# Kernel optimization log

Hardware: AMD Instinct MI355X
Metric: run time of the kernel (lower is better)

The kernel has to match this reference:

```python
import jax, jax.numpy as jnp
import numpy as np

B, N, F_NODE = 4, 50000, 64
E = 1600000
C, F_COL = 1000, 32
H = 16


def setup_inputs() -> dict:
    key = jax.random.key(0)
    ks = jax.random.split(key, 16)
    s = 0.1
    return {
        "node_features": jax.random.normal(ks[0], (B, N, F_NODE), jnp.float32),
        "col_features": jax.random.normal(ks[1], (B, C, F_COL), jnp.float32),
        "edge_index": jax.random.randint(ks[2], (2, E), 0, N, jnp.int32),
        "W1": jax.random.normal(ks[3], (F_NODE, H), jnp.float32) * s,
        "b1": jnp.zeros((H,), jnp.float32),
        "W2": jax.random.normal(ks[4], (H, H), jnp.float32) * s,
        "b2": jnp.zeros((H,), jnp.float32),
        "node_fc_W": jax.random.normal(ks[5], (H, 1), jnp.float32) * s,
        "node_fc_b": jnp.zeros((1,), jnp.float32),
        "col_W1": jax.random.normal(ks[6], (F_COL, H), jnp.float32) * s,
        "col_b1": jnp.zeros((H,), jnp.float32),
        "col_W2": jax.random.normal(ks[7], (H, 1), jnp.float32) * s,
        "col_b2": jnp.zeros((1,), jnp.float32),
        "fc_W": jax.random.normal(ks[8], (2, H), jnp.float32) * s,
        "fc_b": jnp.zeros((H,), jnp.float32),
        "out_W": jax.random.normal(ks[9], (H, 1), jnp.float32) * s,
        "out_b": jnp.zeros((1,), jnp.float32),
    }


def _gcn_conv(x, src, dst, W, b, num_nodes):
    # PyG GCNConv: x' = D^-1/2 (A+I) D^-1/2 (x W) + b
    x = x @ W
    loops = jnp.arange(num_nodes, dtype=src.dtype)
    s = jnp.concatenate([src, loops])
    d = jnp.concatenate([dst, loops])
    deg = jax.ops.segment_sum(jnp.ones_like(d, x.dtype), d, num_segments=num_nodes)
    dinv = jnp.where(deg > 0, jax.lax.rsqrt(deg), 0.0)
    norm = dinv[s] * dinv[d]                     # [E']
    msg = x[s] * norm[:, None]                   # gather + scale
    out = jax.ops.segment_sum(msg, d, num_segments=num_nodes)  # scatter-add
    return out + b


def reference(node_features, col_features, edge_index, W1, b1, W2, b2,
              node_fc_W, node_fc_b, col_W1, col_b1, col_W2, col_b2,
              fc_W, fc_b, out_W, out_b):
    Bs, Nn, Fn = node_features.shape
    num_nodes = Bs * Nn
    x = node_features.reshape(num_nodes, Fn)
    # faithful to torch: edge_index.expand(B,2,E).reshape(2,-1) (indices NOT offset per batch)
    Ee = edge_index.shape[1]
    ei = jnp.broadcast_to(edge_index, (Bs, 2, Ee)).reshape(2, Bs * Ee)
    src, dst = ei[0], ei[1]
    x = jax.nn.relu(_gcn_conv(x, src, dst, W1, b1, num_nodes))
    x = jax.nn.relu(_gcn_conv(x, src, dst, W2, b2, num_nodes))
    x = x.reshape(Bs, Nn, -1)
    node_out = (x @ node_fc_W + node_fc_b)[..., 0]          # [B, N]
    h = jax.nn.relu(col_features @ col_W1 + col_b1)
    col_out = (h @ col_W2 + col_b2)[..., 0]                 # [B, C]
    node_avg = node_out.mean(axis=1)[:, None]               # [B, 1]
    col_avg = col_out.mean(axis=1)[:, None]                 # [B, 1]
    combined = jnp.concatenate([node_avg, col_avg], axis=1)  # [B, 2]
    z = jax.nn.relu(combined @ fc_W + fc_b)
    return z @ out_W + out_b                                # [B, 1]
```

## Files before the change

kernel.cpp:

```cpp
#include <hip/hip_runtime.h>

static constexpr int NN   = 50000;
static constexpr int NBAT = 4;
static constexpr int NE   = 1600000;
static constexpr int NC   = 1000;
static constexpr int FN   = 64;
static constexpr int FCOL = 32;
static constexpr int HD   = 16;

static constexpr int NP     = 20;
static constexpr int PNODES = 2500;
static constexpr int PCAP   = 88000;
static constexpr int NSUB   = 1000;
static constexpr int SNODES = 50;
static constexpr int SCAP   = 2048;
static constexpr int SPP    = 50;
static constexpr int SLICES = 44;
static constexpr int CHUNK  = 4096;
static constexpr int CHUNK2 = 2048;

static constexpr int P1B  = (NE + CHUNK - 1) / CHUNK;
static constexpr int MLPB = (NN + 127) / 128;
static constexpr int COLB = 16;
static constexpr int MEGAB = P1B + NBAT * MLPB + COLB;

__device__ inline float block_reduce_256(float v) {
    __shared__ float s[4];
    int lane = threadIdx.x & 63, wid = threadIdx.x >> 6;
    #pragma unroll
    for (int o = 32; o > 0; o >>= 1) v += __shfl_down(v, o);
    if (lane == 0) s[wid] = v;
    __syncthreads();
    if (threadIdx.x == 0) {
        float t = 0.f;
        #pragma unroll
        for (int i = 0; i < 4; i++) t += s[i];
        return t;
    }
    return 0.f;
}

__device__ inline float dot4(float4 a, float4 w) {
    return (a.x * w.x + a.y * w.y) + (a.z * w.z + a.w * w.w);
}

__device__ inline float4 quad_reduce_scatter(const float (&p)[16], int q) {
    constexpr int KA[8] = {0,1,2,3,8,9,10,11};
    constexpr int KB[8] = {4,5,6,7,12,13,14,15};
    bool hi1 = (q & 1);
    float m[8];
    #pragma unroll
    for (int i = 0; i < 8; i++) {
        float send = hi1 ? p[KA[i]] : p[KB[i]];
        float recv = __shfl_xor(send, 1);
        m[i] = (hi1 ? p[KB[i]] : p[KA[i]]) + recv;
    }
    bool hi2 = (q & 2);
    float s0 = hi2 ? m[0] : m[4];
    float s1 = hi2 ? m[1] : m[5];
    float s2 = hi2 ? m[2] : m[6];
    float s3 = hi2 ? m[3] : m[7];
    float v0 = __shfl_xor(s0, 2);
    float v1 = __shfl_xor(s1, 2);
    float v2 = __shfl_xor(s2, 2);
    float v3 = __shfl_xor(s3, 2);
    return make_float4((hi2 ? m[4] : m[0]) + v0, (hi2 ? m[5] : m[1]) + v1,
                       (hi2 ? m[6] : m[2]) + v2, (hi2 ? m[7] : m[3]) + v3);
}

__device__ inline float mlp_tail(float4 t, int q, bool valid, const float* sw2,
                                 float4 bv, float4 b2v, float4 nfv) {
    float h0 = fmaxf(t.x + bv.x, 0.f);
    float h1 = fmaxf(t.y + bv.y, 0.f);
    float h2 = fmaxf(t.z + bv.z, 0.f);
    float h3 = fmaxf(t.w + bv.w, 0.f);
    float pk[16];
    const float* r0p = &sw2[(q * 4 + 0) * 20];
    const float* r1p = &sw2[(q * 4 + 1) * 20];
    const float* r2p = &sw2[(q * 4 + 2) * 20];
    const float* r3p = &sw2[(q * 4 + 3) * 20];
    #pragma unroll
    for (int k4 = 0; k4 < 4; k4++) {
        float4 w0 = *(const float4*)&r0p[k4 * 4];
        float4 w1 = *(const float4*)&r1p[k4 * 4];
        float4 w2 = *(const float4*)&r2p[k4 * 4];
        float4 w3 = *(const float4*)&r3p[k4 * 4];
        pk[k4*4+0] = h0 * w0.x + h1 * w1.x + h2 * w2.x + h3 * w3.x;
        pk[k4*4+1] = h0 * w0.y + h1 * w1.y + h2 * w2.y + h3 * w3.y;
        pk[k4*4+2] = h0 * w0.z + h1 * w1.z + h2 * w2.z + h3 * w3.z;
        pk[k4*4+3] = h0 * w0.w + h1 * w1.w + h2 * w2.w + h3 * w3.w;
    }
    float4 f = quad_reduce_scatter(pk, q);
    float sv = fmaxf(f.x + b2v.x, 0.f) * nfv.x
             + fmaxf(f.y + b2v.y, 0.f) * nfv.y
             + fmaxf(f.z + b2v.z, 0.f) * nfv.z
             + fmaxf(f.w + b2v.w, 0.f) * nfv.w;
    return valid ? sv : 0.f;
}

__global__ void __launch_bounds__(256) k_mega(
        const float* __restrict__ x, const int* __restrict__ src,
        const int* __restrict__ dst, const float* __restrict__ col,
        const float* __restrict__ W1, const float* __restrict__ b1,
        const float* __restrict__ W2, const float* __restrict__ b2,
        const float* __restrict__ nfcW,
        const float* __restrict__ cW1, const float* __restrict__ cb1,
        const float* __restrict__ cW2,
        int* __restrict__ gcur, unsigned* __restrict__ buf1,
        float* __restrict__ y1, double* __restrict__ sums) {
    __shared__ int ph[NP], pg[NP], pl[NP];
    __shared__ float swt[HD * FN];
    __shared__ float sw2[HD * 20];
    __shared__ float sb1[HD], sb2[HD], snf[HD];
    __shared__ float cw1s[FCOL * HD], csb1[HD], csw2[HD];

    int tid = threadIdx.x;
    int idx = blockIdx.x;
    int i5 = idx / 5, r5 = idx - i5 * 5;
    bool isP1 = (r5 == 0) && (i5 < P1B);

    if (isP1) {
        if (tid < NP) ph[tid] = 0;
        __syncthreads();
        int e0 = i5 * CHUNK;
        unsigned ent[16]; int bin[16];
        #pragma unroll
        for (int k = 0; k < 16; k++) {
            int e = e0 + k * 256 + tid;
            if (e < NE) {
                unsigned d = (unsigned)dst[e], s = (unsigned)src[e];
                ent[k] = (d << 16) | s;
                bin[k] = (int)(d / (unsigned)PNODES);
                atomicAdd(&ph[bin[k]], 1);
            } else bin[k] = -1;
        }
        __syncthreads();
        if (tid < NP) { pg[tid] = atomicAdd(&gcur[tid], ph[tid]); pl[tid] = 0; }
        __syncthreads();
        #pragma unroll
        for (int k = 0; k < 16; k++) {
            if (bin[k] >= 0) {
                int p = pg[bin[k]] + atomicAdd(&pl[bin[k]], 1);
                if (p < PCAP) buf1[(size_t)bin[k] * PCAP + p] = ent[k];
            }
        }
        return;
    }

    int p1below = (i5 < P1B) ? (i5 + (r5 > 0 ? 1 : 0)) : P1B;
    int rank = idx - p1below;

    if (rank < NBAT * MLPB) {
        int b = rank / MLPB, nb = rank - b * MLPB;
        int q = tid & 3;
        int n0 = nb * 128 + (tid >> 2) * 2;
        bool v0 = (n0 < NN), v1 = (n0 + 1 < NN);
        const float* xb = x + (size_t)b * NN * FN;

        float4 a0, a1, a2, a3, c0, c1, c2, c3;
        a0 = a1 = a2 = a3 = c0 = c1 = c2 = c3 = make_float4(0.f, 0.f, 0.f, 0.f);
        if (v0) {
            const float4* p = (const float4*)(xb + (size_t)n0 * FN + q * 16);
            a0 = p[0]; a1 = p[1]; a2 = p[2]; a3 = p[3];
        }
        if (v1) {
            const float4* p = (const float4*)(xb + (size_t)(n0 + 1) * FN + q * 16);
            c0 = p[0]; c1 = p[1]; c2 = p[2]; c3 = p[3];
        }

        #pragma unroll
        for (int i = tid; i < HD * FN; i += 256) {
            int j = i >> 6, k = i & 63;
            swt[i] = W1[k * HD + j];
        }
        if (tid < HD * HD) sw2[(tid >> 4) * 20 + (tid & 15)] = W2[tid];
        if (tid < HD) { sb1[tid] = b1[tid]; sb2[tid] = b2[tid]; snf[tid] = nfcW[tid]; }
        __syncthreads();

        float p0[16], p1[16];
        #pragma unroll
        for (int j = 0; j < HD; j++) {
            const float4* w = (const float4*)&swt[j * FN + q * 16];
            float4 w0 = w[0], w1 = w[1], w2 = w[2], w3 = w[3];
            p0[j] = (dot4(a0, w0) + dot4(a1, w1)) + (dot4(a2, w2) + dot4(a3, w3));
            p1[j] = (dot4(c0, w0) + dot4(c1, w1)) + (dot4(c2, w2) + dot4(c3, w3));
        }
        float4 r0 = quad_reduce_scatter(p0, q);
        float4 r1 = quad_reduce_scatter(p1, q);

        if (b == 0) {
            if (v0) *(float4*)&y1[(size_t)n0 * HD + q * 4] = r0;
            if (v1) *(float4*)&y1[(size_t)(n0 + 1) * HD + q * 4] = r1;
        } else {
            float4 bv  = *(const float4*)&sb1[q * 4];
            float4 b2v = *(const float4*)&sb2[q * 4];
            float4 nfv = *(const float4*)&snf[q * 4];
            float sv = mlp_tail(r0, q, v0, sw2, bv, b2v, nfv)
                     + mlp_tail(r1, q, v1, sw2, bv, b2v, nfv);
            float bs = block_reduce_256(sv);
            if (tid == 0) atomicAdd(&sums[b], (double)bs);
        }
        return;
    }

    {
        int t = rank - NBAT * MLPB;
        int b = t & 3, chunk = t >> 2;
        for (int i = tid; i < FCOL * HD; i += 256) cw1s[i] = cW1[i];
        if (tid < HD) { csb1[tid] = cb1[tid]; csw2[tid] = cW2[tid]; }
        __syncthreads();
        int c = chunk * 256 + tid;
        float sv = 0.f;
        if (c < NC) {
            const float4* cf = (const float4*)(col + ((size_t)b * NC + c) * FCOL);
            float h[HD];
            #pragma unroll
            for (int j = 0; j < HD; j++) h[j] = csb1[j];
            #pragma unroll
            for (int k4 = 0; k4 < FCOL / 4; k4++) {
                float4 f = cf[k4];
                #pragma unroll
                for (int j = 0; j < HD; j++) {
                    h[j] += f.x * cw1s[(4 * k4 + 0) * HD + j];
                    h[j] += f.y * cw1s[(4 * k4 + 1) * HD + j];
                    h[j] += f.z * cw1s[(4 * k4 + 2) * HD + j];
                    h[j] += f.w * cw1s[(4 * k4 + 3) * HD + j];
                }
            }
            #pragma unroll
            for (int j = 0; j < HD; j++) sv += fmaxf(h[j], 0.f) * csw2[j];
        }
        float bs = block_reduce_256(sv);
        if (tid == 0) atomicAdd(&sums[4 + b], (double)bs);
    }
}

__global__ void __launch_bounds__(256) k_part2(
        const int* __restrict__ gcur, const unsigned* __restrict__ buf1,
        int* __restrict__ cur2, unsigned* __restrict__ buf2) {
    __shared__ int hist[SPP], gbase[SPP], lcur[SPP];
    int part = blockIdx.x / SLICES;
    int slice = blockIdx.x % SLICES;
    int count = min(gcur[part], PCAP);
    int base = slice * CHUNK2;
    if (base >= count) return;
    const unsigned* in = buf1 + (size_t)part * PCAP;
    int sub0 = part * SPP;
    int tid = threadIdx.x;
    if (tid < SPP) hist[tid] = 0;
    __syncthreads();
    unsigned ent[8]; int bin[8];
    #pragma unroll
    for (int k = 0; k < 8; k++) {
        int i = base + k * 256 + tid;
        if (i < count) {
            unsigned e = in[i];
            ent[k] = e;
            bin[k] = (int)((e >> 16) / (unsigned)SNODES) - sub0;
            atomicAdd(&hist[bin[k]], 1);
        } else bin[k] = -1;
    }
    __syncthreads();
    if (tid < SPP) { gbase[tid] = atomicAdd(&cur2[sub0 + tid], hist[tid]); lcur[tid] = 0; }
    __syncthreads();
    #pragma unroll
    for (int k = 0; k < 8; k++) {
        if (bin[k] >= 0) {
            int p = gbase[bin[k]] + atomicAdd(&lcur[bin[k]], 1);
            if (p < SCAP) buf2[(size_t)(sub0 + bin[k]) * SCAP + p] = ent[k];
        }
    }
}

__global__ void __launch_bounds__(256) k_hist(
        const int* __restrict__ cur2, const unsigned* __restrict__ buf2,
        int* __restrict__ cnt, float* __restrict__ dinv, float* __restrict__ z1) {
    __shared__ int hist[SNODES];
    int tid = threadIdx.x, sub = blockIdx.x, vbase = sub * SNODES;
    if (tid < SNODES) hist[tid] = 0;
    __syncthreads();
    int count = min(cur2[sub], SCAP);
    const unsigned* in = buf2 + (size_t)sub * SCAP;
    for (int i = tid; i < count; i += 256)
        atomicAdd(&hist[(int)(in[i] >> 16) - vbase], 1);
    __syncthreads();
    if (tid < SNODES) {
        int c = hist[tid];
        cnt[vbase + tid] = c;
        dinv[vbase + tid] = rsqrtf((float)(4 * c + 1));
    }
    __syncthreads();
    if (tid < SNODES * 4) {
        int vl = tid >> 2, f4 = tid & 3;
        float dv = rsqrtf((float)(4 * hist[vl] + 1));
        float4* p = (float4*)&z1[(size_t)(vbase + vl) * HD + f4 * 4];
        float4 v = *p;
        *p = make_float4(dv * v.x, dv * v.y, dv * v.z, dv * v.w);
    }
}

__device__ inline void sort_sublist(int sub, const int* __restrict__ cur2,
                                    const int* __restrict__ cnt,
                                    const unsigned* __restrict__ buf2,
                                    unsigned* sorted, int* rp, int* cur, int* s) {
    int tid = threadIdx.x, vbase = sub * SNODES;
    int own = (tid < SNODES) ? cnt[vbase + tid] : 0;
    if (tid < 64) s[tid] = own;
    __syncthreads();
    #pragma unroll
    for (int off = 1; off < 64; off <<= 1) {
        int v = (tid < 64 && tid >= off) ? s[tid - off] : 0;
        __syncthreads();
        if (tid < 64) s[tid] += v;
        __syncthreads();
    }
    if (tid < SNODES) {
        int excl = s[tid] - own;
        rp[tid] = excl;
        cur[tid] = excl;
    }
    if (tid == SNODES - 1) rp[SNODES] = s[tid];
    __syncthreads();
    int count = min(cur2[sub], SCAP);
    const unsigned* in = buf2 + (size_t)sub * SCAP;
    for (int i = tid; i < count; i += 256) {
        unsigned e = in[i];
        int p = atomicAdd(&cur[(int)(e >> 16) - vbase], 1);
        sorted[p] = e;
    }
    __syncthreads();
}

__device__ inline void load_sorted(int sub, const int* __restrict__ cur2,
                                   const int* __restrict__ cnt,
                                   const unsigned* __restrict__ buf2,
                                   unsigned* sorted, int* rp, int* s) {
    int tid = threadIdx.x, vbase = sub * SNODES;
    int own = (tid < SNODES) ? cnt[vbase + tid] : 0;
    if (tid < 64) s[tid] = own;
    __syncthreads();
    #pragma unroll
    for (int off = 1; off < 64; off <<= 1) {
        int v = (tid < 64 && tid >= off) ? s[tid - off] : 0;
        __syncthreads();
        if (tid < 64) s[tid] += v;
        __syncthreads();
    }
    if (tid < SNODES) rp[tid] = s[tid] - own;
    if (tid == SNODES - 1) rp[SNODES] = s[tid];
    __syncthreads();
    int count = min(cur2[sub], SCAP);
    const unsigned* in = buf2 + (size_t)sub * SCAP;
    for (int i = tid; i < count; i += 256) sorted[i] = in[i];
    __syncthreads();
}

__device__ inline float gather_run(const unsigned* sorted, int s0, int s1,
                                   const float* __restrict__ z, int j) {
    float acc = 0.f;
    int i = s0;
    for (; i + 8 <= s1; i += 8) {
        unsigned e0 = sorted[i],   e1 = sorted[i+1], e2 = sorted[i+2], e3 = sorted[i+3];
        unsigned e4 = sorted[i+4], e5 = sorted[i+5], e6 = sorted[i+6], e7 = sorted[i+7];
        float v0 = z[(e0 & 0xffffu) * HD + j];
        float v1 = z[(e1 & 0xffffu) * HD + j];
        float v2 = z[(e2 & 0xffffu) * HD + j];
        float v3 = z[(e3 & 0xffffu) * HD + j];
        float v4 = z[(e4 & 0xffffu) * HD + j];
        float v5 = z[(e5 & 0xffffu) * HD + j];
        float v6 = z[(e6 & 0xffffu) * HD + j];
        float v7 = z[(e7 & 0xffffu) * HD + j];
        acc += ((v0 + v1) + (v2 + v3)) + ((v4 + v5) + (v6 + v7));
    }
    for (; i + 4 <= s1; i += 4) {
        unsigned a = sorted[i], b = sorted[i+1], c = sorted[i+2], d = sorted[i+3];
        float va = z[(a & 0xffffu) * HD + j];
        float vb = z[(b & 0xffffu) * HD + j];
        float vc = z[(c & 0xffffu) * HD + j];
        float vd = z[(d & 0xffffu) * HD + j];
        acc += (va + vb) + (vc + vd);
    }
    for (; i < s1; i++) acc += z[(sorted[i] & 0xffffu) * HD + j];
    return acc;
}

__global__ void __launch_bounds__(256) k_conv1(
        const int* __restrict__ cur2, const int* __restrict__ cnt,
        unsigned* __restrict__ buf2,
        const float* __restrict__ dinv, const float* __restrict__ z1,
        const float* __restrict__ b1, const float* __restrict__ W2,
        float* __restrict__ z2) {
    __shared__ unsigned sorted[SCAP];
    __shared__ int rp[SNODES + 1], cur[SNODES], s[64];
    __shared__ float sW[HD * HD], sb[HD];
    int tid = threadIdx.x;
    if (tid < HD * HD) sW[tid] = W2[tid];
    if (tid < HD) sb[tid] = b1[tid];
    int sub = blockIdx.x, vbase = sub * SNODES;
    sort_sublist(sub, cur2, cnt, buf2, sorted, rp, cur, s);

    {
        int count = min(cur2[sub], SCAP);
        unsigned* outp = buf2 + (size_t)sub * SCAP;
        for (int i = tid; i < count; i += 256) outp[i] = sorted[i];
    }

    int j = tid & 15, g = tid >> 4;
    int sbase = (tid & 63) & 48;
    #pragma unroll
    for (int it = 0; it < (SNODES + 15) / 16; it++) {
        int lv = it * 16 + g;
        bool valid = (lv < SNODES);
        float h = 0.f, dv = 0.f;
        if (valid) {
            float acc = gather_run(sorted, rp[lv], rp[lv + 1], z1, j);
            int v = vbase + lv;
            dv = dinv[v];
            h = fmaxf(4.f * dv * acc + dv * z1[v * HD + j] + sb[j], 0.f);
        }
        float o = 0.f;
        #pragma unroll
        for (int k = 0; k < HD; k++) o += __shfl(h, sbase + k) * sW[k * HD + j];
        if (valid) z2[(vbase + lv) * HD + j] = dv * o;
    }
}

__global__ void __launch_bounds__(256) k_conv2(
        const int* __restrict__ cur2, const int* __restrict__ cnt,
        const unsigned* __restrict__ buf2,
        const float* __restrict__ dinv, const float* __restrict__ z2,
        const float* __restrict__ b2, const float* __restrict__ nfcW,
        double* __restrict__ sums) {
    __shared__ unsigned sorted[SCAP];
    __shared__ int rp[SNODES + 1], s[64];
    __shared__ float sb[HD], sw[HD];
    int tid = threadIdx.x;
    if (tid < HD) { sb[tid] = b2[tid]; sw[tid] = nfcW[tid]; }
    int sub = blockIdx.x, vbase = sub * SNODES;
    load_sorted(sub, cur2, cnt, buf2, sorted, rp, s);

    int j = tid & 15, g = tid >> 4;
    float part = 0.f;
    #pragma unroll
    for (int it = 0; it < (SNODES + 15) / 16; it++) {
        int lv = it * 16 + g;
        if (lv < SNODES) {
            float acc = gather_run(sorted, rp[lv], rp[lv + 1], z2, j);
            int v = vbase + lv;
            float dv = dinv[v];
            float h = fmaxf(4.f * dv * acc + dv * z2[v * HD + j] + sb[j], 0.f);
            part += h * sw[j];
        }
    }
    float bs = block_reduce_256(part);
    if (tid == 0) atomicAdd(&sums[0], (double)bs);
}

__global__ void k_final(const double* __restrict__ sums,
                        const float* __restrict__ nfcb, const float* __restrict__ cb2,
                        const float* __restrict__ fcW, const float* __restrict__ fcb,
                        const float* __restrict__ outW, const float* __restrict__ outb,
                        float* __restrict__ out) {
    int b = threadIdx.x;
    if (b < NBAT) {
        float na = (float)(sums[b] * (1.0 / NN)) + nfcb[0];
        float ca = (float)(sums[4 + b] * (1.0 / NC)) + cb2[0];
        float o = outb[0];
        #pragma unroll
        for (int j = 0; j < HD; j++) {
            float z = fmaxf(na * fcW[j] + ca * fcW[HD + j] + fcb[j], 0.f);
            o += z * outW[j];
        }
        out[b] = o;
    }
}

extern "C" void kernel_launch(void* const* d_in, const int* in_sizes, int n_in,
                              void* d_out, int out_size, void* d_ws, size_t ws_size,
                              hipStream_t stream) {
    const float* x    = (const float*)d_in[0];
    const float* col  = (const float*)d_in[1];
    const int*   ei   = (const int*)d_in[2];
    const float* W1   = (const float*)d_in[3];
    const float* b1   = (const float*)d_in[4];
    const float* W2   = (const float*)d_in[5];
    const float* b2   = (const float*)d_in[6];
    const float* nfcW = (const float*)d_in[7];
    const float* nfcb = (const float*)d_in[8];
    const float* cW1  = (const float*)d_in[9];
    const float* cb1  = (const float*)d_in[10];
    const float* cW2  = (const float*)d_in[11];
    const float* cb2  = (const float*)d_in[12];
    const float* fcW  = (const float*)d_in[13];
    const float* fcb  = (const float*)d_in[14];
    const float* outW = (const float*)d_in[15];
    const float* outb = (const float*)d_in[16];
    float* out = (float*)d_out;

    char* ws = (char*)d_ws;
    int*      gcur = (int*)     (ws + 0);
    int*      cur2 = (int*)     (ws + 128);
    double*   sums = (double*)  (ws + 4160);
    int*      cnt  = (int*)     (ws + 4224);
    float*    dinv = (float*)   (ws + 204224);
    unsigned* buf1 = (unsigned*)(ws + 404480);
    float*    z2   = (float*)   (ws + 404480);
    float*    z1   = (float*)   (ws + 7444480);
    unsigned* buf2 = (unsigned*)(ws + 10644480);

    const int* src = ei;
    const int* dst = ei + NE;

    hipMemsetAsync(gcur, 0, 4224, stream);

    k_mega <<<MEGAB, 256, 0, stream>>>(x, src, dst, col, W1, b1, W2, b2,
                                       nfcW, cW1, cb1, cW2, gcur, buf1, z1, sums);
    k_part2<<<NP * SLICES, 256, 0, stream>>>(gcur, buf1, cur2, buf2);
    k_hist <<<NSUB, 256, 0, stream>>>(cur2, buf2, cnt, dinv, z1);
    k_conv1<<<NSUB, 256, 0, stream>>>(cur2, cnt, buf2, dinv, z1, b1, W2, z2);
    k_conv2<<<NSUB, 256, 0, stream>>>(cur2, cnt, buf2, dinv, z2, b2, nfcW, sums);
    k_final<<<1, 64, 0, stream>>>(sums, nfcb, cb2, fcW, fcb, outW, outb, out);
}
```

Baseline: 103.8 us.

## Process four node tiles per MLP block with software-prefetched loads

Each MLP block in the fused mega-kernel now handles four 128-node tiles instead of one. It prefetches the next tile's node features into registers while computing the current one, and accumulates the per-batch sum across tiles before a single block reduction and atomic. The block interleaving pattern changes from 1-in-5 to 1-in-2 for partition blocks, matching the smaller number of MLP blocks. The aim is to amortize the weight staging and atomics over more nodes and to hide load latency, at the cost of higher register pressure and fewer, longer blocks.

```diff
diff --git a/kernel.cpp b/kernel.cpp
--- a/kernel.cpp
+++ b/kernel.cpp
@@ -19,10 +19,11 @@
 static constexpr int CHUNK  = 4096;
 static constexpr int CHUNK2 = 2048;
 
-static constexpr int P1B  = (NE + CHUNK - 1) / CHUNK;
-static constexpr int MLPB = (NN + 127) / 128;
-static constexpr int COLB = 16;
-static constexpr int MEGAB = P1B + NBAT * MLPB + COLB;
+static constexpr int P1B   = (NE + CHUNK - 1) / CHUNK;
+static constexpr int NIT   = 4;
+static constexpr int MLPB4 = 98;
+static constexpr int COLB  = 16;
+static constexpr int MEGAB = P1B + NBAT * MLPB4 + COLB;
 
 __device__ inline float block_reduce_256(float v) {
     __shared__ float s[4];
@@ -116,13 +117,13 @@
 
     int tid = threadIdx.x;
     int idx = blockIdx.x;
-    int i5 = idx / 5, r5 = idx - i5 * 5;
-    bool isP1 = (r5 == 0) && (i5 < P1B);
+    int i2 = idx >> 1, r2 = idx & 1;
+    bool isP1 = (r2 == 0) && (i2 < P1B);
 
     if (isP1) {
         if (tid < NP) ph[tid] = 0;
         __syncthreads();
-        int e0 = i5 * CHUNK;
+        int e0 = i2 * CHUNK;
         unsigned ent[16]; int bin[16];
         #pragma unroll
         for (int k = 0; k < 16; k++) {
@@ -147,25 +148,27 @@
         return;
     }
 
-    int p1below = (i5 < P1B) ? (i5 + (r5 > 0 ? 1 : 0)) : P1B;
+    int p1below = min(i2 + r2, P1B);
     int rank = idx - p1below;
 
-    if (rank < NBAT * MLPB) {
-        int b = rank / MLPB, nb = rank - b * MLPB;
+    if (rank < NBAT * MLPB4) {
+        int b = rank / MLPB4, nb = rank - b * MLPB4;
         int q = tid & 3;
-        int n0 = nb * 128 + (tid >> 2) * 2;
-        bool v0 = (n0 < NN), v1 = (n0 + 1 < NN);
+        int nrow = (tid >> 2) * 2;
         const float* xb = x + (size_t)b * NN * FN;
 
         float4 a0, a1, a2, a3, c0, c1, c2, c3;
         a0 = a1 = a2 = a3 = c0 = c1 = c2 = c3 = make_float4(0.f, 0.f, 0.f, 0.f);
-        if (v0) {
-            const float4* p = (const float4*)(xb + (size_t)n0 * FN + q * 16);
-            a0 = p[0]; a1 = p[1]; a2 = p[2]; a3 = p[3];
-        }
-        if (v1) {
-            const float4* p = (const float4*)(xb + (size_t)(n0 + 1) * FN + q * 16);
-            c0 = p[0]; c1 = p[1]; c2 = p[2]; c3 = p[3];
+        {
+            int n0 = (nb * NIT + 0) * 128 + nrow;
+            if (n0 < NN) {
+                const float4* p = (const float4*)(xb + (size_t)n0 * FN + q * 16);
+                a0 = p[0]; a1 = p[1]; a2 = p[2]; a3 = p[3];
+            }
+            if (n0 + 1 < NN) {
+                const float4* p = (const float4*)(xb + (size_t)(n0 + 1) * FN + q * 16);
+                c0 = p[0]; c1 = p[1]; c2 = p[2]; c3 = p[3];
+            }
         }
 
         #pragma unroll
@@ -177,34 +180,61 @@
         if (tid < HD) { sb1[tid] = b1[tid]; sb2[tid] = b2[tid]; snf[tid] = nfcW[tid]; }
         __syncthreads();
 
-        float p0[16], p1[16];
-        #pragma unroll
-        for (int j = 0; j < HD; j++) {
-            const float4* w = (const float4*)&swt[j * FN + q * 16];
-            float4 w0 = w[0], w1 = w[1], w2 = w[2], w3 = w[3];
-            p0[j] = (dot4(a0, w0) + dot4(a1, w1)) + (dot4(a2, w2) + dot4(a3, w3));
-            p1[j] = (dot4(c0, w0) + dot4(c1, w1)) + (dot4(c2, w2) + dot4(c3, w3));
-        }
-        float4 r0 = quad_reduce_scatter(p0, q);
-        float4 r1 = quad_reduce_scatter(p1, q);
-
-        if (b == 0) {
-            if (v0) *(float4*)&y1[(size_t)n0 * HD + q * 4] = r0;
-            if (v1) *(float4*)&y1[(size_t)(n0 + 1) * HD + q * 4] = r1;
-        } else {
-            float4 bv  = *(const float4*)&sb1[q * 4];
-            float4 b2v = *(const float4*)&sb2[q * 4];
-            float4 nfv = *(const float4*)&snf[q * 4];
-            float sv = mlp_tail(r0, q, v0, sw2, bv, b2v, nfv)
-                     + mlp_tail(r1, q, v1, sw2, bv, b2v, nfv);
-            float bs = block_reduce_256(sv);
+        float4 bv  = *(const float4*)&sb1[q * 4];
+        float4 b2v = *(const float4*)&sb2[q * 4];
+        float4 nfv = *(const float4*)&snf[q * 4];
+        float svacc = 0.f;
+
+        #pragma unroll
+        for (int it = 0; it < NIT; ++it) {
+            int n0 = (nb * NIT + it) * 128 + nrow;
+            bool v0 = (n0 < NN), v1 = (n0 + 1 < NN);
+
+            float4 na0, na1, na2, na3, nc0, nc1, nc2, nc3;
+            na0 = na1 = na2 = na3 = nc0 = nc1 = nc2 = nc3 = make_float4(0.f, 0.f, 0.f, 0.f);
+            if (it < NIT - 1) {
+                int m0 = n0 + 128;
+                if (m0 < NN) {
+                    const float4* p = (const float4*)(xb + (size_t)m0 * FN + q * 16);
+                    na0 = p[0]; na1 = p[1]; na2 = p[2]; na3 = p[3];
+                }
+                if (m0 + 1 < NN) {
+                    const float4* p = (const float4*)(xb + (size_t)(m0 + 1) * FN + q * 16);
+                    nc0 = p[0]; nc1 = p[1]; nc2 = p[2]; nc3 = p[3];
+                }
+            }
+
+            float p0[16], p1[16];
+            #pragma unroll
+            for (int j = 0; j < HD; j++) {
+                const float4* w = (const float4*)&swt[j * FN + q * 16];
+                float4 w0 = w[0], w1 = w[1], w2 = w[2], w3 = w[3];
+                p0[j] = (dot4(a0, w0) + dot4(a1, w1)) + (dot4(a2, w2) + dot4(a3, w3));
+                p1[j] = (dot4(c0, w0) + dot4(c1, w1)) + (dot4(c2, w2) + dot4(c3, w3));
+            }
+            float4 r0 = quad_reduce_scatter(p0, q);
+            float4 r1 = quad_reduce_scatter(p1, q);
+
+            if (b == 0) {
+                if (v0) *(float4*)&y1[(size_t)n0 * HD + q * 4] = r0;
+                if (v1) *(float4*)&y1[(size_t)(n0 + 1) * HD + q * 4] = r1;
+            } else {
+                svacc += mlp_tail(r0, q, v0, sw2, bv, b2v, nfv)
+                       + mlp_tail(r1, q, v1, sw2, bv, b2v, nfv);
+            }
+
+            a0 = na0; a1 = na1; a2 = na2; a3 = na3;
+            c0 = nc0; c1 = nc1; c2 = nc2; c3 = nc3;
+        }
+        if (b != 0) {
+            float bs = block_reduce_256(svacc);
             if (tid == 0) atomicAdd(&sums[b], (double)bs);
         }
         return;
     }
 
     {
-        int t = rank - NBAT * MLPB;
+        int t = rank - NBAT * MLPB4;
         int b = t & 3, chunk = t >> 2;
         for (int i = tid; i < FCOL * HD; i += 256) cw1s[i] = cW1[i];
         if (tid < HD) { csb1[tid] = cb1[tid]; csw2[tid] = cW2[tid]; }
```

After: 162.0 us. 1.56x slower.
